# Kernel optimization log

Measured on AMD Instinct MI355X. Metric: run time of the kernel, lower is better.

The kernel has to match this reference:

```python
import jax, jax.numpy as jnp
import numpy as np

SH_C0 = 0.28209479177387814
SH_C1 = 0.4886025119029199
EPS2D = 0.3  # gsplat 'classic' rasterize_mode adds 0.3 to 2D covariance diagonal
NEAR_PLANE = 0.01
FAR_PLANE = 1e10
ALPHA_MIN = 1.0 / 255.0
ALPHA_MAX = 0.999
T_EPS = 1e-4  # gsplat terminates compositing when transmittance drops below this

N_GAUSS = 2048
WIDTH = 160
HEIGHT = 160


def _quat_to_rotmat(q):
    q = q / jnp.linalg.norm(q, axis=-1, keepdims=True)
    w, x, y, z = q[:, 0], q[:, 1], q[:, 2], q[:, 3]
    return jnp.stack([
        1 - 2 * (y * y + z * z), 2 * (x * y - w * z), 2 * (x * z + w * y),
        2 * (x * y + w * z), 1 - 2 * (x * x + z * z), 2 * (y * z - w * x),
        2 * (x * z - w * y), 2 * (y * z + w * x), 1 - 2 * (x * x + y * y),
    ], axis=-1).reshape(-1, 3, 3)


def _forward(means3d, opacities, scales, quats, sh0, shN, camtoworlds, Ks, width, height):
    viewmat = jnp.linalg.inv(camtoworlds)[0]  # world->cam, single camera
    K = Ks[0]
    fx, fy, cx, cy = K[0, 0], K[1, 1], K[0, 2], K[1, 2]
    opac = jax.nn.sigmoid(opacities)
    sh = jnp.concatenate([sh0, shN], axis=1)  # [N,4,3]

    # degree-1 SH -> view-dependent RGB
    campos = camtoworlds[0, :3, 3]
    d = means3d - campos
    d = d / jnp.linalg.norm(d, axis=-1, keepdims=True)
    dxv, dyv, dzv = d[:, 0:1], d[:, 1:2], d[:, 2:3]
    colors = SH_C0 * sh[:, 0] + SH_C1 * (-dyv * sh[:, 1] + dzv * sh[:, 2] - dxv * sh[:, 3]) + 0.5
    colors = jnp.maximum(colors, 0.0)  # [N,3]

    # 3D covariance = R S S^T R^T
    R = _quat_to_rotmat(quats)
    M = R * scales[:, None, :]
    cov3d = M @ jnp.swapaxes(M, 1, 2)  # [N,3,3]

    # project to camera
    W3, t3 = viewmat[:3, :3], viewmat[:3, 3]
    tcam = means3d @ W3.T + t3  # [N,3]
    tz = tcam[:, 2]
    rz = 1.0 / tz
    lim_x = 1.3 * (0.5 * width / fx)
    lim_y = 1.3 * (0.5 * height / fy)
    txz = jnp.clip(tcam[:, 0] * rz, -lim_x, lim_x)
    tyz = jnp.clip(tcam[:, 1] * rz, -lim_y, lim_y)
    zero = jnp.zeros_like(rz)
    J = jnp.stack([
        jnp.stack([fx * rz, zero, -fx * txz * rz], axis=-1),
        jnp.stack([zero, fy * rz, -fy * tyz * rz], axis=-1),
    ], axis=-2)  # [N,2,3]
    cov_cam = jnp.einsum('ij,njk,lk->nil', W3, cov3d, W3)
    cov2d = jnp.einsum('nij,njk,nlk->nil', J, cov_cam, J)  # [N,2,2]
    a = cov2d[:, 0, 0] + EPS2D
    bb = cov2d[:, 0, 1]
    c = cov2d[:, 1, 1] + EPS2D
    det = a * c - bb * bb
    det_safe = jnp.where(det > 0, det, 1.0)
    cA, cB, cC = c / det_safe, -bb / det_safe, a / det_safe  # conic
    mx = fx * tcam[:, 0] * rz + cx
    my = fy * tcam[:, 1] * rz + cy
    valid = (tz > NEAR_PLANE) & (tz < FAR_PLANE) & (det > 0)

    # global front-to-back depth sort (single camera)
    order = jnp.argsort(tz)
    mx, my = mx[order], my[order]
    cA, cB, cC = cA[order], cB[order], cC[order]
    opac_s, colors_s = opac[order], colors[order]
    tz_s, valid_s = tz[order], valid[order]

    # pixel centers, flattened row-major [P = H*W]
    xs = jnp.arange(width, dtype=means3d.dtype) + 0.5
    ys = jnp.arange(height, dtype=means3d.dtype) + 0.5
    px = jnp.tile(xs, height)
    py = jnp.repeat(ys, width)

    dx = px[:, None] - mx[None, :]  # [P,N]
    dy = py[:, None] - my[None, :]
    sigma = 0.5 * (cA[None, :] * dx * dx + cC[None, :] * dy * dy) + cB[None, :] * dx * dy
    alpha = jnp.minimum(ALPHA_MAX, opac_s[None, :] * jnp.exp(-sigma))
    keep = valid_s[None, :] & (sigma >= 0) & (alpha >= ALPHA_MIN)
    alpha = jnp.where(keep, alpha, 0.0)

    T = jnp.cumprod(1.0 - alpha, axis=-1)
    T_excl = jnp.concatenate([jnp.ones_like(T[:, :1]), T[:, :-1]], axis=-1)
    w = jnp.where(T_excl > T_EPS, alpha * T_excl, 0.0)  # [P,N]

    rgb = w @ colors_s                     # [P,3]
    depth = w @ tz_s                       # [P] accumulated depth
    alpha_tot = jnp.sum(w, axis=-1)        # [P]
    ed = depth / jnp.maximum(alpha_tot, 1e-10)  # expected depth ('ED')
    render_colors = jnp.concatenate([rgb, ed[:, None]], axis=-1).reshape(1, height, width, 4)
    render_alphas = alpha_tot.reshape(1, height, width, 1)
    return render_colors, render_alphas


def setup_inputs() -> dict:
    key = jax.random.key(0)
    ks = jax.random.split(key, 6)
    means3d = jax.random.normal(ks[0], (N_GAUSS, 3), jnp.float32) * 1.0 + jnp.array([0.0, 0.0, 4.0])
    opacities = jax.random.normal(ks[1], (N_GAUSS,), jnp.float32)
    scales = jax.random.uniform(ks[2], (N_GAUSS, 3), jnp.float32) * 0.05 + 0.01
    quats = jax.random.normal(ks[3], (N_GAUSS, 4), jnp.float32)
    sh0 = jax.random.normal(ks[4], (N_GAUSS, 1, 3), jnp.float32) * 0.5
    shN = jax.random.normal(ks[5], (N_GAUSS, 3, 3), jnp.float32) * 0.1
    camtoworlds = jnp.eye(4, dtype=jnp.float32)[None]  # camera at origin looking +z
    Ks = jnp.array([[[200.0, 0.0, WIDTH / 2.0], [0.0, 200.0, HEIGHT / 2.0], [0.0, 0.0, 1.0]]], jnp.float32)
    return {"means3d": means3d, "opacities": opacities, "scales": scales, "quats": quats,
            "sh0": sh0, "shN": shN, "camtoworlds": camtoworlds, "Ks": Ks,
            "width": WIDTH, "height": HEIGHT}


def reference(means3d, opacities, scales, quats, sh0, shN, camtoworlds, Ks, width, height):
    return _forward(means3d, opacities, scales, quats, sh0, shN, camtoworlds, Ks, width, height)
```

## Files before the change

### kernel.cpp

```cpp
#include <hip/hip_runtime.h>
#include <math.h>

#define SH_C0f 0.28209479177387814f
#define SH_C1f 0.4886025119029199f
#define EPS2D 0.3f
#define NEAR_PLANE 0.01f
#define FAR_PLANE 1e10f
#define ALPHA_MIN (1.0f/255.0f)
#define ALPHA_MAX 0.999f
#define T_EPS 1e-4f
#define TS 8
#define NW 8

__global__ void preprocess_kernel(
    const float* __restrict__ means, const float* __restrict__ opac_in,
    const float* __restrict__ scales, const float* __restrict__ quats,
    const float* __restrict__ sh0, const float* __restrict__ shN,
    const float* __restrict__ c2w, const float* __restrict__ Ks,
    const int* __restrict__ wptr, const int* __restrict__ hptr,
    float4* __restrict__ attrs, float4* __restrict__ bounds, int N)
{
    int i = blockIdx.x * blockDim.x + threadIdx.x;
    if (i >= N) return;

    float m[16];
    #pragma unroll
    for (int k = 0; k < 16; k++) m[k] = c2w[k];
    float inv[12];
    inv[0]  =  m[5]*m[10]*m[15] - m[5]*m[11]*m[14] - m[9]*m[6]*m[15] + m[9]*m[7]*m[14] + m[13]*m[6]*m[11] - m[13]*m[7]*m[10];
    inv[4]  = -m[4]*m[10]*m[15] + m[4]*m[11]*m[14] + m[8]*m[6]*m[15] - m[8]*m[7]*m[14] - m[12]*m[6]*m[11] + m[12]*m[7]*m[10];
    inv[8]  =  m[4]*m[9]*m[15]  - m[4]*m[11]*m[13] - m[8]*m[5]*m[15] + m[8]*m[7]*m[13] + m[12]*m[5]*m[11] - m[12]*m[7]*m[9];
    inv[1]  = -m[1]*m[10]*m[15] + m[1]*m[11]*m[14] + m[9]*m[2]*m[15] - m[9]*m[3]*m[14] - m[13]*m[2]*m[11] + m[13]*m[3]*m[10];
    inv[5]  =  m[0]*m[10]*m[15] - m[0]*m[11]*m[14] - m[8]*m[2]*m[15] + m[8]*m[3]*m[14] + m[12]*m[2]*m[11] - m[12]*m[3]*m[10];
    inv[9]  = -m[0]*m[9]*m[15]  + m[0]*m[11]*m[13] + m[8]*m[1]*m[15] - m[8]*m[3]*m[13] - m[12]*m[1]*m[11] + m[12]*m[3]*m[9];
    inv[2]  =  m[1]*m[6]*m[15]  - m[1]*m[7]*m[14]  - m[5]*m[2]*m[15] + m[5]*m[3]*m[14] + m[13]*m[2]*m[7]  - m[13]*m[3]*m[6];
    inv[6]  = -m[0]*m[6]*m[15]  + m[0]*m[7]*m[14]  + m[4]*m[2]*m[15] - m[4]*m[3]*m[14] - m[12]*m[2]*m[7]  + m[12]*m[3]*m[6];
    inv[10] =  m[0]*m[5]*m[15]  - m[0]*m[7]*m[13]  - m[4]*m[1]*m[15] + m[4]*m[3]*m[13] + m[12]*m[1]*m[7]  - m[12]*m[3]*m[5];
    inv[3]  = -m[1]*m[6]*m[11]  + m[1]*m[7]*m[10]  + m[5]*m[2]*m[11] - m[5]*m[3]*m[10] - m[9]*m[2]*m[7]   + m[9]*m[3]*m[6];
    inv[7]  =  m[0]*m[6]*m[11]  - m[0]*m[7]*m[10]  - m[4]*m[2]*m[11] + m[4]*m[3]*m[10] + m[8]*m[2]*m[7]   - m[8]*m[3]*m[6];
    inv[11] = -m[0]*m[5]*m[11]  + m[0]*m[7]*m[9]   + m[4]*m[1]*m[11] - m[4]*m[3]*m[9]  - m[8]*m[1]*m[7]   + m[8]*m[3]*m[5];
    {
        float inv12 = -m[4]*m[9]*m[14] + m[4]*m[10]*m[13] + m[8]*m[5]*m[14] - m[8]*m[6]*m[13] - m[12]*m[5]*m[10] + m[12]*m[6]*m[9];
        float det = m[0]*inv[0] + m[1]*inv[4] + m[2]*inv[8] + m[3]*inv12;
        float r = 1.0f / det;
        #pragma unroll
        for (int k = 0; k < 12; k++) inv[k] *= r;
    }
    const float W00 = inv[0], W01 = inv[1], W02 = inv[2],  t0 = inv[3];
    const float W10 = inv[4], W11 = inv[5], W12 = inv[6],  t1 = inv[7];
    const float W20 = inv[8], W21 = inv[9], W22 = inv[10], t2 = inv[11];

    const float fx = Ks[0], cx = Ks[2], fy = Ks[4], cy = Ks[5];
    const float width = (float)wptr[0], height = (float)hptr[0];

    const float mxx = means[i*3+0], myy = means[i*3+1], mzz = means[i*3+2];

    const float cpx = m[3], cpy = m[7], cpz = m[11];
    float dx = mxx - cpx, dy = myy - cpy, dz = mzz - cpz;
    float dn = sqrtf(dx*dx + dy*dy + dz*dz);
    dx /= dn; dy /= dn; dz /= dn;

    float col[3];
    #pragma unroll
    for (int c = 0; c < 3; c++) {
        float v = SH_C0f * sh0[i*3+c]
                + SH_C1f * (-dy * shN[i*9 + 0*3 + c] + dz * shN[i*9 + 1*3 + c] - dx * shN[i*9 + 2*3 + c])
                + 0.5f;
        col[c] = fmaxf(v, 0.0f);
    }

    const float op = 1.0f / (1.0f + expf(-opac_in[i]));

    float qw = quats[i*4+0], qx = quats[i*4+1], qy = quats[i*4+2], qz = quats[i*4+3];
    float qn = sqrtf(qw*qw + qx*qx + qy*qy + qz*qz);
    qw /= qn; qx /= qn; qy /= qn; qz /= qn;
    const float R00 = 1.f - 2.f*(qy*qy + qz*qz), R01 = 2.f*(qx*qy - qw*qz), R02 = 2.f*(qx*qz + qw*qy);
    const float R10 = 2.f*(qx*qy + qw*qz), R11 = 1.f - 2.f*(qx*qx + qz*qz), R12 = 2.f*(qy*qz - qw*qx);
    const float R20 = 2.f*(qx*qz - qw*qy), R21 = 2.f*(qy*qz + qw*qx), R22 = 1.f - 2.f*(qx*qx + qy*qy);

    const float sx = scales[i*3+0], sy = scales[i*3+1], sz = scales[i*3+2];
    const float M00 = R00*sx, M01 = R01*sy, M02 = R02*sz;
    const float M10 = R10*sx, M11 = R11*sy, M12 = R12*sz;
    const float M20 = R20*sx, M21 = R21*sy, M22 = R22*sz;

    const float S00 = M00*M00 + M01*M01 + M02*M02;
    const float S01 = M00*M10 + M01*M11 + M02*M12;
    const float S02 = M00*M20 + M01*M21 + M02*M22;
    const float S11 = M10*M10 + M11*M11 + M12*M12;
    const float S12 = M10*M20 + M11*M21 + M12*M22;
    const float S22 = M20*M20 + M21*M21 + M22*M22;

    const float tcx = W00*mxx + W01*myy + W02*mzz + t0;
    const float tcy = W10*mxx + W11*myy + W12*mzz + t1;
    const float tcz = W20*mxx + W21*myy + W22*mzz + t2;
    const float rz = 1.0f / tcz;

    const float limx = 1.3f * (0.5f * width / fx);
    const float limy = 1.3f * (0.5f * height / fy);
    const float txz = fminf(fmaxf(tcx * rz, -limx), limx);
    const float tyz = fminf(fmaxf(tcy * rz, -limy), limy);

    const float V00 = W00*S00 + W01*S01 + W02*S02;
    const float V01 = W00*S01 + W01*S11 + W02*S12;
    const float V02 = W00*S02 + W01*S12 + W02*S22;
    const float V10 = W10*S00 + W11*S01 + W12*S02;
    const float V11 = W10*S01 + W11*S11 + W12*S12;
    const float V12 = W10*S02 + W11*S12 + W12*S22;
    const float V20 = W20*S00 + W21*S01 + W22*S02;
    const float V21 = W20*S01 + W21*S11 + W22*S12;
    const float V22 = W20*S02 + W21*S12 + W22*S22;
    const float CC00 = V00*W00 + V01*W01 + V02*W02;
    const float CC01 = V00*W10 + V01*W11 + V02*W12;
    const float CC02 = V00*W20 + V01*W21 + V02*W22;
    const float CC11 = V10*W10 + V11*W11 + V12*W12;
    const float CC12 = V10*W20 + V11*W21 + V12*W22;
    const float CC22 = V20*W20 + V21*W21 + V22*W22;

    const float j00 = fx * rz,  j02 = -fx * txz * rz;
    const float j11 = fy * rz,  j12 = -fy * tyz * rz;

    const float u0 = j00*CC00 + j02*CC02;
    const float u1 = j00*CC01 + j02*CC12;
    const float u2 = j00*CC02 + j02*CC22;
    const float v1 = j11*CC11 + j12*CC12;
    const float v2 = j11*CC12 + j12*CC22;
    const float c2d00 = u0*j00 + u2*j02;
    const float c2d01 = u1*j11 + u2*j12;
    const float c2d11 = v1*j11 + v2*j12;

    const float a  = c2d00 + EPS2D;
    const float bb = c2d01;
    const float cc = c2d11 + EPS2D;
    const float det = a*cc - bb*bb;
    const float det_safe = (det > 0.0f) ? det : 1.0f;
    const float invd = 1.0f / det_safe;

    const bool valid = (tcz > NEAR_PLANE) && (tcz < FAR_PLANE) && (det > 0.0f);

    float rad = 0.0f;
    if (valid && op >= ALPHA_MIN) {
        const float lmax = 0.5f*(a + cc) + sqrtf(fmaxf(0.f, 0.25f*(a - cc)*(a - cc) + bb*bb));
        const float sig_cut = logf(255.0f * op);
        rad = sqrtf(fmaxf(sig_cut, 0.0f) * 2.0f * lmax) * 1.001f + 0.5f;
    }

    const float mx2d = fx * tcx * rz + cx;
    const float my2d = fy * tcy * rz + cy;

    attrs[i*3+0] = make_float4(mx2d, my2d, 0.5f * cc * invd, -bb * invd);
    attrs[i*3+1] = make_float4(0.5f * a * invd, op, tcz, rad);
    attrs[i*3+2] = make_float4(col[0], col[1], col[2], 0.0f);
    bounds[i]   = make_float4(mx2d, my2d, rad, 0.0f);
}

__device__ __forceinline__ float eval_alpha(const float4 g0, const float4 g1,
                                            const float px, const float py) {
    const float ddx = px - g0.x;
    const float ddy = py - g0.y;
    const float sg = g0.z*ddx*ddx + g1.x*ddy*ddy + g0.w*ddx*ddy;
    float a = g1.y * expf(-sg);
    return ((sg >= 0.0f) && (a >= ALPHA_MIN)) ? fminf(a, ALPHA_MAX) : 0.0f;
}

__global__ __launch_bounds__(512) void raster_kernel(
    const float4* __restrict__ attrs, const float4* __restrict__ bounds,
    float* __restrict__ out, int N, int P, const int* __restrict__ wptr)
{
    extern __shared__ int smem[];
    int*   s_list   = smem;
    float* s_keys   = (float*)(smem + N);
    int*   s_sorted = smem + 2*N;
    __shared__ int   s_wcnt[NW];
    __shared__ float s_P[NW][64];
    __shared__ float s_red[NW][64][5];

    const int width  = wptr[0];
    const int height = P / width;
    const int tilesX = (width  + TS - 1) / TS;
    const int tilesY = (height + TS - 1) / TS;
    const int nTiles = tilesX * tilesY;
    const int tid  = threadIdx.x;
    const int lane = tid & 63;
    const int wv   = tid >> 6;

    for (int tile = blockIdx.x; tile < nTiles; tile += gridDim.x) {
        __syncthreads();

        const int tx = tile % tilesX, ty = tile / tilesX;
        const float x0 = (float)(tx*TS) + 0.5f;
        const float x1 = (float)(min(tx*TS + TS - 1, width  - 1)) + 0.5f;
        const float y0 = (float)(ty*TS) + 0.5f;
        const float y1 = (float)(min(ty*TS + TS - 1, height - 1)) + 0.5f;

        int count = 0;
        for (int base = 0; base < N; base += 512) {
            const int j = base + tid;
            bool pred = false;
            if (j < N) {
                const float4 b = bounds[j];
                pred = (b.z > 0.0f) &&
                       (b.x + b.z >= x0) && (b.x - b.z <= x1) &&
                       (b.y + b.z >= y0) && (b.y - b.z <= y1);
            }
            const unsigned long long m = __ballot(pred);
            const int pre = __popcll(m & ((1ull << lane) - 1ull));
            if (lane == 0) s_wcnt[wv] = (int)__popcll(m);
            __syncthreads();
            int off = count + pre;
            int tot = 0;
            #pragma unroll
            for (int w = 0; w < NW; w++) {
                if (w < wv) off += s_wcnt[w];
                tot += s_wcnt[w];
            }
            if (pred) s_list[off] = j;
            count += tot;
            __syncthreads();
        }

        for (int t = tid; t < count; t += 512)
            s_keys[t] = attrs[s_list[t]*3 + 1].z;
        __syncthreads();
        for (int t = tid; t < count; t += 512) {
            const float kt = s_keys[t];
            int rank = 0;
            for (int mIdx = 0; mIdx < count; mIdx++) {
                const float km = s_keys[mIdx];
                rank += (km < kt) || (km == kt && mIdx < t);
            }
            s_sorted[rank] = s_list[t];
        }
        __syncthreads();

        const int px_i = tx*TS + (lane & (TS-1));
        const int py_i = ty*TS + (lane >> 3);
        const bool active = (px_i < width) && (py_i < height);
        const float px = (float)px_i + 0.5f;
        const float py = (float)py_i + 0.5f;

        const int seg    = (count + NW - 1) / NW;
        const int cstart = wv * seg;
        const int cend   = min(cstart + seg, count);

        float Tl = 1.0f;
        float accr = 0.f, accg = 0.f, accb = 0.f, accd = 0.f, acca = 0.f;
        for (int p = cstart; p < cend; p += 4) {
            int id[4];
            float al[4];
            float4 G1[4], G2[4];
            #pragma unroll
            for (int u = 0; u < 4; u++)
                id[u] = s_sorted[(p+u < cend) ? (p+u) : p];
            #pragma unroll
            for (int u = 0; u < 4; u++) {
                const int idx = __builtin_amdgcn_readfirstlane(id[u]);
                const float4 g0 = attrs[idx*3+0];
                G1[u] = attrs[idx*3+1];
                G2[u] = attrs[idx*3+2];
                const float a = eval_alpha(g0, G1[u], px, py);
                al[u] = (p+u < cend) ? a : 0.0f;
            }
            #pragma unroll
            for (int u = 0; u < 4; u++) {
                const float w = al[u] * Tl;
                accr += w * G2[u].x;
                accg += w * G2[u].y;
                accb += w * G2[u].z;
                accd += w * G1[u].z;
                acca += w;
                Tl *= (1.0f - al[u]);
            }
            if (__all(Tl <= T_EPS)) break;
        }
        s_P[wv][lane] = Tl;
        __syncthreads();

        float Ts = active ? 1.0f : 0.0f;
        for (int m = 0; m < wv; m++) Ts *= s_P[m][lane];

        s_red[wv][lane][0] = accr * Ts;
        s_red[wv][lane][1] = accg * Ts;
        s_red[wv][lane][2] = accb * Ts;
        s_red[wv][lane][3] = accd * Ts;
        s_red[wv][lane][4] = acca * Ts;
        __syncthreads();

        if (wv == 0 && active) {
            float r = 0.f, g = 0.f, b = 0.f, d = 0.f, a = 0.f;
            #pragma unroll
            for (int m = 0; m < NW; m++) {
                r += s_red[m][lane][0];
                g += s_red[m][lane][1];
                b += s_red[m][lane][2];
                d += s_red[m][lane][3];
                a += s_red[m][lane][4];
            }
            const int pix = py_i * width + px_i;
            out[pix*4 + 0] = r;
            out[pix*4 + 1] = g;
            out[pix*4 + 2] = b;
            out[pix*4 + 3] = d / fmaxf(a, 1e-10f);
            out[(size_t)P*4 + pix] = a;
        }
    }
}

extern "C" void kernel_launch(void* const* d_in, const int* in_sizes, int n_in,
                              void* d_out, int out_size, void* d_ws, size_t ws_size,
                              hipStream_t stream) {
    const float* means   = (const float*)d_in[0];
    const float* opac    = (const float*)d_in[1];
    const float* scales  = (const float*)d_in[2];
    const float* quats   = (const float*)d_in[3];
    const float* sh0     = (const float*)d_in[4];
    const float* shN     = (const float*)d_in[5];
    const float* c2w     = (const float*)d_in[6];
    const float* Ks      = (const float*)d_in[7];
    const int*   wptr    = (const int*)d_in[8];
    const int*   hptr    = (const int*)d_in[9];

    const int N = in_sizes[0] / 3;
    const int P = out_size / 5;

    float4* attrs  = (float4*)d_ws;
    float4* bounds = attrs + 3*N;

    const int gb = (N + 255) / 256;
    hipLaunchKernelGGL(preprocess_kernel, dim3(gb), dim3(256), 0, stream,
                       means, opac, scales, quats, sh0, shN, c2w, Ks, wptr, hptr,
                       attrs, bounds, N);

    const size_t lds = (size_t)3 * N * sizeof(int);
    hipLaunchKernelGGL(raster_kernel, dim3(512), dim3(512), lds, stream,
                       attrs, bounds, (float*)d_out, N, P, wptr);
}
```

Measured before the change: 20.63 us.

## Cull per-wave slices without block barriers and rank-sort using depths in bounds

Each wave now culls its own contiguous slice of gaussians with a ballot and local prefix, which removes the two block-wide barriers per 512-gaussian chunk. Depth is packed into the bounds record, so the sort no longer gathers keys from attrs. Ranking iterates over per-wave compacted slices and breaks ties by gaussian index. Block size doubles to 1024 threads (16 waves), which raises per-block LDS for the reduction arrays and may lower occupancy.

```diff
diff --git a/kernel.cpp b/kernel.cpp
--- a/kernel.cpp
+++ b/kernel.cpp
@@ -10,7 +10,7 @@
 #define ALPHA_MAX 0.999f
 #define T_EPS 1e-4f
 #define TS 8
-#define NW 8
+#define NW 16
 
 __global__ void preprocess_kernel(
     const float* __restrict__ means, const float* __restrict__ opac_in,
@@ -150,7 +150,7 @@
     attrs[i*3+0] = make_float4(mx2d, my2d, 0.5f * cc * invd, -bb * invd);
     attrs[i*3+1] = make_float4(0.5f * a * invd, op, tcz, rad);
     attrs[i*3+2] = make_float4(col[0], col[1], col[2], 0.0f);
-    bounds[i]   = make_float4(mx2d, my2d, rad, 0.0f);
+    bounds[i]   = make_float4(mx2d, my2d, rad, tcz);
 }
 
 __device__ __forceinline__ float eval_alpha(const float4 g0, const float4 g1,
@@ -162,15 +162,16 @@
     return ((sg >= 0.0f) && (a >= ALPHA_MIN)) ? fminf(a, ALPHA_MAX) : 0.0f;
 }
 
-__global__ __launch_bounds__(512) void raster_kernel(
+__global__ __launch_bounds__(1024) void raster_kernel(
     const float4* __restrict__ attrs, const float4* __restrict__ bounds,
     float* __restrict__ out, int N, int P, const int* __restrict__ wptr)
 {
     extern __shared__ int smem[];
-    int*   s_list   = smem;
-    float* s_keys   = (float*)(smem + N);
-    int*   s_sorted = smem + 2*N;
-    __shared__ int   s_wcnt[NW];
+    const int SLICE = (N + NW - 1) / NW;
+    int*   s_idx    = smem;
+    float* s_tz     = (float*)(smem + NW*SLICE);
+    int*   s_sorted = smem + 2*NW*SLICE;
+    __shared__ int   s_cnt[NW];
     __shared__ float s_P[NW][64];
     __shared__ float s_red[NW][64][5];
 
@@ -192,43 +193,65 @@
         const float y0 = (float)(ty*TS) + 0.5f;
         const float y1 = (float)(min(ty*TS + TS - 1, height - 1)) + 0.5f;
 
+        {
+            const int sstart = wv * SLICE;
+            const int send   = min(sstart + SLICE, N);
+            int cnt = 0;
+            for (int base = sstart; base < send; base += 64) {
+                const int j = base + lane;
+                bool pred = false;
+                float tzv = 0.0f;
+                if (j < send) {
+                    const float4 b = bounds[j];
+                    tzv = b.w;
+                    pred = (b.z > 0.0f) &&
+                           (b.x + b.z >= x0) && (b.x - b.z <= x1) &&
+                           (b.y + b.z >= y0) && (b.y - b.z <= y1);
+                }
+                const unsigned long long m = __ballot(pred);
+                const int pre = __popcll(m & ((1ull << lane) - 1ull));
+                if (pred) {
+                    s_idx[sstart + cnt + pre] = j;
+                    s_tz [sstart + cnt + pre] = tzv;
+                }
+                cnt += (int)__popcll(m);
+            }
+            if (lane == 0) s_cnt[wv] = cnt;
+        }
+        __syncthreads();
+
         int count = 0;
-        for (int base = 0; base < N; base += 512) {
-            const int j = base + tid;
-            bool pred = false;
-            if (j < N) {
-                const float4 b = bounds[j];
-                pred = (b.z > 0.0f) &&
-                       (b.x + b.z >= x0) && (b.x - b.z <= x1) &&
-                       (b.y + b.z >= y0) && (b.y - b.z <= y1);
-            }
-            const unsigned long long m = __ballot(pred);
-            const int pre = __popcll(m & ((1ull << lane) - 1ull));
-            if (lane == 0) s_wcnt[wv] = (int)__popcll(m);
-            __syncthreads();
-            int off = count + pre;
-            int tot = 0;
-            #pragma unroll
-            for (int w = 0; w < NW; w++) {
-                if (w < wv) off += s_wcnt[w];
-                tot += s_wcnt[w];
-            }
-            if (pred) s_list[off] = j;
-            count += tot;
-            __syncthreads();
-        }
-
-        for (int t = tid; t < count; t += 512)
-            s_keys[t] = attrs[s_list[t]*3 + 1].z;
-        __syncthreads();
-        for (int t = tid; t < count; t += 512) {
-            const float kt = s_keys[t];
-            int rank = 0;
-            for (int mIdx = 0; mIdx < count; mIdx++) {
-                const float km = s_keys[mIdx];
-                rank += (km < kt) || (km == kt && mIdx < t);
-            }
-            s_sorted[rank] = s_list[t];
+        #pragma unroll
+        for (int w = 0; w < NW; w++) count += s_cnt[w];
+
+        {
+            const int sstart = wv * SLICE;
+            const int mycnt  = s_cnt[wv];
+            for (int e = lane; e < mycnt; e += 64) {
+                const float tze = s_tz[sstart + e];
+                const int   ide = s_idx[sstart + e];
+                int rank = 0;
+                #pragma unroll 1
+                for (int w2 = 0; w2 < NW; w2++) {
+                    const int b2 = w2 * SLICE;
+                    const int c2 = s_cnt[w2];
+                    int p2 = 0;
+                    for (; p2 + 3 < c2; p2 += 4) {
+                        #pragma unroll
+                        for (int u = 0; u < 4; u++) {
+                            const float t2 = s_tz[b2 + p2 + u];
+                            const int   i2 = s_idx[b2 + p2 + u];
+                            rank += (t2 < tze) || (t2 == tze && i2 < ide);
+                        }
+                    }
+                    for (; p2 < c2; p2++) {
+                        const float t2 = s_tz[b2 + p2];
+                        const int   i2 = s_idx[b2 + p2];
+                        rank += (t2 < tze) || (t2 == tze && i2 < ide);
+                    }
+                }
+                s_sorted[rank] = ide;
+            }
         }
         __syncthreads();
 
@@ -330,7 +353,8 @@
                        means, opac, scales, quats, sh0, shN, c2w, Ks, wptr, hptr,
                        attrs, bounds, N);
 
-    const size_t lds = (size_t)3 * N * sizeof(int);
-    hipLaunchKernelGGL(raster_kernel, dim3(512), dim3(512), lds, stream,
+    const int SLICE = (N + NW - 1) / NW;
+    const size_t lds = (size_t)(2 * NW * SLICE + N) * sizeof(int);
+    hipLaunchKernelGGL(raster_kernel, dim3(512), dim3(1024), lds, stream,
                        attrs, bounds, (float*)d_out, N, P, wptr);
 }
```

Result: slower. 29.32 us (+42.1%).
